# Kernel tuning notes

Measured on AMD Instinct MI355X. Metric: run time of the kernel, lower is better.

Reference implementation:

```python
import jax, jax.numpy as jnp
import numpy as np


def rotate_half(x):
    x1, x2 = jnp.split(x, 2, axis=-1)
    return jnp.concatenate((-x2, x1), axis=-1)


def setup_inputs() -> dict:
    key = jax.random.key(0)
    ks = jax.random.split(key, 8)
    B, S, H, C = 4, 2048, 2048, 512
    QK = H + C
    NH = 16
    dqk = QK // NH  # 160
    return {
        "hidden_states": jax.random.normal(ks[0], (B, S, H), jnp.float32),
        "cond_states": jax.random.normal(ks[1], (B, S, C), jnp.float32),
        "cos": jax.random.uniform(ks[2], (S, dqk), jnp.float32),
        "sin": jax.random.uniform(ks[3], (S, dqk), jnp.float32),
        "Wq": jax.random.normal(ks[4], (QK, QK), jnp.float32) * 0.02,
        "Wk": jax.random.normal(ks[5], (QK, QK), jnp.float32) * 0.02,
        "Wv": jax.random.normal(ks[6], (H, H), jnp.float32) * 0.02,
        "Wo": jax.random.normal(ks[7], (H, H), jnp.float32) * 0.02,
    }


def reference(hidden_states, cond_states, cos, sin, Wq, Wk, Wv, Wo):
    B, S, H = hidden_states.shape
    NH = 16
    qk_in = jnp.concatenate([hidden_states, cond_states], axis=-1)  # [B,S,QK]
    q = (qk_in @ Wq.T).reshape(B, S, NH, -1)  # [B,S,NH,dqk]
    k = (qk_in @ Wk.T).reshape(B, S, NH, -1)
    v = (hidden_states @ Wv.T).reshape(B, S, NH, -1)  # [B,S,NH,dv]
    # RoPE in fp32; cos/sin broadcast over batch and heads: (S,1,dqk)
    cos_b = cos[:, None, :].astype(jnp.float32)
    sin_b = sin[:, None, :].astype(jnp.float32)
    qf, kf = q.astype(jnp.float32), k.astype(jnp.float32)
    q = (qf * cos_b + rotate_half(qf) * sin_b).astype(q.dtype)
    k = (kf * cos_b + rotate_half(kf) * sin_b).astype(k.dtype)
    dqk = q.shape[-1]
    scale = 1.0 / jnp.sqrt(jnp.asarray(dqk, q.dtype))
    scores = jnp.einsum("bqhd,bkhd->bhqk", q, k) * scale  # [B,NH,S,S]
    probs = jax.nn.softmax(scores, axis=-1)
    attn = jnp.einsum("bhqk,bkhd->bqhd", probs, v)  # [B,S,NH,dv]
    attn = attn.reshape(B, S, -1)
    return attn @ Wo.T
```

## Files before the change

### kernel.cpp

```cpp
#include <hip/hip_runtime.h>
#include <cstdint>
#include <cstddef>

typedef __attribute__((ext_vector_type(8))) short bf16x8;
typedef __attribute__((ext_vector_type(4))) short bf16x4;
typedef __attribute__((ext_vector_type(4))) float f32x4;

#define MFMA_BF16 __builtin_amdgcn_mfma_f32_16x16x32_bf16

constexpr int B_   = 4;
constexpr int S_   = 2048;
constexpr int H_   = 2048;
constexpr int C_   = 512;
constexpr int QKD  = 2560;
constexpr int NH   = 16;
constexpr int DQK  = 160;
constexpr int DV   = 128;
constexpr int MTOT = B_ * S_;

static __device__ __forceinline__ short f2bf(float f) {
  unsigned u = __builtin_bit_cast(unsigned, f);
  u += 0x7FFFu + ((u >> 16) & 1u);
  return (short)(u >> 16);
}
static __device__ __forceinline__ float bf2f(short h) {
  unsigned u = ((unsigned)(unsigned short)h) << 16;
  return __builtin_bit_cast(float, u);
}
static __device__ __forceinline__ unsigned cvt_pk_bf16(float a, float b) {
  unsigned r;
  asm("v_cvt_pk_bf16_f32 %0, %1, %2" : "=v"(r) : "v"(a), "v"(b));
  return r;
}
static __device__ __forceinline__ void gload_lds16(const void* g, void* l) {
  __builtin_amdgcn_global_load_lds((const __attribute__((address_space(1))) unsigned*)g,
                                   (__attribute__((address_space(3))) unsigned*)l, 16, 0, 0);
}

__global__ __launch_bounds__(256) void k_build_qkin(const float* __restrict__ hidden,
                                                    const float* __restrict__ cond,
                                                    short* __restrict__ qk) {
  int i = blockIdx.x * 256 + threadIdx.x;
  int row = i / (QKD / 4);
  int c4  = i - row * (QKD / 4);
  f32x4 v;
  if (c4 < H_ / 4) v = *((const f32x4*)hidden + (size_t)row * (H_ / 4) + c4);
  else             v = *((const f32x4*)cond   + (size_t)row * (C_ / 4) + (c4 - H_ / 4));
  bf16x4 o;
  o[0] = f2bf(v[0]); o[1] = f2bf(v[1]); o[2] = f2bf(v[2]); o[3] = f2bf(v[3]);
  *(bf16x4*)(qk + (size_t)row * QKD + c4 * 4) = o;
}

__global__ __launch_bounds__(256) void k_cvt_bf16(const float* __restrict__ in,
                                                  short* __restrict__ out) {
  size_t i = (size_t)blockIdx.x * 256 + threadIdx.x;
  f32x4 v = *((const f32x4*)in + i);
  bf16x4 o;
  o[0] = f2bf(v[0]); o[1] = f2bf(v[1]); o[2] = f2bf(v[2]); o[3] = f2bf(v[3]);
  *(bf16x4*)(out + i * 4) = o;
}

template<int MODE>
__global__ __launch_bounds__(256) void k_gemm_bt(const short* __restrict__ A,
                                                 const short* __restrict__ W,
                                                 void* __restrict__ Cp,
                                                 int N, int K, int lda) {
  __shared__ short lA[128 * 32];
  __shared__ short lB[128 * 32];
  const int tid = threadIdx.x;
  const int lane = tid & 63, wid = tid >> 6;
  const int gx = gridDim.x, gy = gridDim.y;
  const int nwg = gx * gy, cpx = nwg >> 3;
  const int wg  = blockIdx.y * gx + blockIdx.x;
  const int wg2 = (wg & 7) * cpx + (wg >> 3);
  const int xb  = wg2 / gy, yb = wg2 - xb * gy;
  const int m0 = yb * 128, n0 = xb * 128;
  const int wr = wid >> 1, wc = wid & 1;
  const int l15 = lane & 15, l4 = lane >> 4;
  f32x4 acc[4][4] = {};

  const int srow = lane >> 2;
  const int scol = (lane & 3) * 8;
  const short* Abase = A + (size_t)m0 * lda;
  const short* Wbase = W + (size_t)n0 * K;
  const int nkt = K >> 5;

  for (int kt = 0; kt < nkt; ++kt) {
    const int k0 = kt << 5;
#pragma unroll
    for (int i = 0; i < 2; ++i) {
      int c = wid * 2 + i;
      gload_lds16(Abase + (size_t)(c * 16 + srow) * lda + k0 + scol, &lA[c * 512]);
      gload_lds16(Wbase + (size_t)(c * 16 + srow) * K   + k0 + scol, &lB[c * 512]);
    }
    __syncthreads();
    bf16x8 af[4], bv[4];
#pragma unroll
    for (int x = 0; x < 4; ++x) {
      af[x] = *(const bf16x8*)&lA[(wr * 64 + x * 16 + l15) * 32 + l4 * 8];
      bv[x] = *(const bf16x8*)&lB[(wc * 64 + x * 16 + l15) * 32 + l4 * 8];
    }
#pragma unroll
    for (int mi = 0; mi < 4; ++mi)
#pragma unroll
      for (int nj = 0; nj < 4; ++nj)
        acc[mi][nj] = MFMA_BF16(af[mi], bv[nj], acc[mi][nj], 0, 0, 0);
    __syncthreads();
  }

#pragma unroll
  for (int mi = 0; mi < 4; ++mi) {
#pragma unroll
    for (int nj = 0; nj < 4; ++nj) {
      int crow = m0 + wr * 64 + mi * 16 + l4 * 4;
      int ccol = n0 + wc * 64 + nj * 16 + l15;
      if constexpr (MODE == 0) {
        int b = crow >> 11;
        int s = crow - (b << 11);
        int h = ccol / DQK;
        int d = ccol - h * DQK;
        short* dst = (short*)Cp + ((size_t)(b * NH + h) * S_) * DQK + d;
#pragma unroll
        for (int r = 0; r < 4; ++r)
          dst[(size_t)(s + r) * DQK] = f2bf(acc[mi][nj][r]);
      } else if constexpr (MODE == 1) {
        int b = crow >> 11;
        int s = crow - (b << 11);
        int h = ccol >> 7;
        int d = ccol & 127;
        short* dst = (short*)Cp + ((size_t)(b * NH + h) * DV + d) * S_ + s;
        bf16x4 o;
        o[0] = f2bf(acc[mi][nj][0]); o[1] = f2bf(acc[mi][nj][1]);
        o[2] = f2bf(acc[mi][nj][2]); o[3] = f2bf(acc[mi][nj][3]);
        *(bf16x4*)dst = o;
      } else {
        float* dst = (float*)Cp + (size_t)crow * N + ccol;
#pragma unroll
        for (int r = 0; r < 4; ++r) dst[(size_t)r * N] = acc[mi][nj][r];
      }
    }
  }
}

__global__ __launch_bounds__(256) void k_rope(short* __restrict__ x,
                                              const float* __restrict__ cs,
                                              const float* __restrict__ sn) {
  int i = blockIdx.x * 256 + threadIdx.x;
  int c4   = i % 20;
  int rest = i / 20;
  int s  = rest & (S_ - 1);
  int bh = rest >> 11;
  size_t base = ((size_t)bh * S_ + s) * DQK;
  int d = c4 * 4;
  bf16x4 x1 = *(bf16x4*)(x + base + d);
  bf16x4 x2 = *(bf16x4*)(x + base + d + 80);
  f32x4 c1 = *(const f32x4*)(cs + (size_t)s * DQK + d);
  f32x4 s1 = *(const f32x4*)(sn + (size_t)s * DQK + d);
  f32x4 c2 = *(const f32x4*)(cs + (size_t)s * DQK + d + 80);
  f32x4 s2 = *(const f32x4*)(sn + (size_t)s * DQK + d + 80);
  bf16x4 o1, o2;
#pragma unroll
  for (int j = 0; j < 4; ++j) {
    float a = bf2f(x1[j]), b = bf2f(x2[j]);
    o1[j] = f2bf(a * c1[j] - b * s1[j]);
    o2[j] = f2bf(b * c2[j] + a * s2[j]);
  }
  *(bf16x4*)(x + base + d)      = o1;
  *(bf16x4*)(x + base + d + 80) = o2;
}

__global__ __launch_bounds__(256) void k_attn(const short* __restrict__ q,
                                              const short* __restrict__ k,
                                              const short* __restrict__ vt,
                                              short* __restrict__ attn) {
  __shared__ short lK[64 * 160];
  __shared__ short lV[128 * 64];
  __shared__ short lP[4 * 32 * 64];
  const int tid = threadIdx.x, lane = tid & 63, wid = tid >> 6;
  const int wg  = blockIdx.y * gridDim.x + blockIdx.x;
  const int wg2 = (wg & 7) * 128 + (wg >> 3);
  const int bh  = wg2 >> 4, b = bh >> 4, h = bh & 15;
  const int q0  = (wg2 & 15) * 128;
  const short* Q  = q  + (size_t)bh * S_ * DQK;
  const char*  Kb = (const char*)(k + (size_t)bh * S_ * DQK);
  const char*  Vb = (const char*)(vt + (size_t)bh * DV * S_);
  const int l15 = lane & 15, l4 = lane >> 4;

  bf16x8 qf[2][5];
#pragma unroll
  for (int mi = 0; mi < 2; ++mi)
#pragma unroll
    for (int ks = 0; ks < 5; ++ks)
      qf[mi][ks] = *(const bf16x8*)(Q + (size_t)(q0 + wid * 32 + mi * 16 + l15) * DQK + ks * 32 + l4 * 8);

  f32x4 acc[2][8] = {};
  float mrow[2], lrow[2];
#pragma unroll
  for (int mi = 0; mi < 2; ++mi) { mrow[mi] = -1e30f; lrow[mi] = 0.f; }
  const float csc = 0.07905694150420949f * 1.44269504089f;

  int koff[5], kcolS[5];
#pragma unroll
  for (int i = 0; i < 5; ++i) {
    int c = wid * 5 + i;
    int off = c * 1024 + lane * 16;
    int row = off / 320;
    int colB = off - row * 320;
    int g = colB >> 4;
    int colS = (g < 16) ? (colB ^ ((row & 7) << 4)) : (colB ^ ((row & 3) << 4));
    koff[i] = row;  kcolS[i] = colS;
  }

  for (int kv0 = 0; kv0 < S_; kv0 += 64) {
#pragma unroll
    for (int i = 0; i < 5; ++i)
      gload_lds16(Kb + (size_t)(kv0 + koff[i]) * 320 + kcolS[i], &lK[(wid * 5 + i) * 512]);
#pragma unroll
    for (int i = 0; i < 4; ++i) {
      int c = wid * 4 + i;
      int row = c * 8 + (lane >> 3);
      int cb  = (lane & 7) ^ (lane >> 3);
      gload_lds16(Vb + (size_t)row * (S_ * 2) + kv0 * 2 + cb * 16, &lV[c * 512]);
    }
    __syncthreads();

    f32x4 sc[4][2] = {};
#pragma unroll
    for (int kj = 0; kj < 4; ++kj) {
      int row = kj * 16 + l15;
      int x7 = (row & 7) << 4, x3 = (row & 3) << 4;
#pragma unroll
      for (int ks = 0; ks < 5; ++ks) {
        int colB = (ks < 4) ? ((ks * 64 + l4 * 16) ^ x7) : ((256 + l4 * 16) ^ x3);
        bf16x8 kf = *(const bf16x8*)((const char*)lK + row * 320 + colB);
        sc[kj][0] = MFMA_BF16(kf, qf[0][ks], sc[kj][0], 0, 0, 0);
        sc[kj][1] = MFMA_BF16(kf, qf[1][ks], sc[kj][1], 0, 0, 0);
      }
    }

    float pms[2];
#pragma unroll
    for (int mi = 0; mi < 2; ++mi) {
      float mv = sc[0][mi][0];
#pragma unroll
      for (int kj = 0; kj < 4; ++kj)
#pragma unroll
        for (int r = 0; r < 4; ++r) mv = fmaxf(mv, sc[kj][mi][r]);
      mv = fmaxf(mv, __shfl_xor(mv, 16, 64));
      mv = fmaxf(mv, __shfl_xor(mv, 32, 64));
      pms[mi] = mv * csc;
    }
    if (__any((pms[0] > mrow[0] + 8.0f) || (pms[1] > mrow[1] + 8.0f))) {
#pragma unroll
      for (int mi = 0; mi < 2; ++mi) {
        float mn = fmaxf(mrow[mi], pms[mi]);
        float al = exp2f(mrow[mi] - mn);
        mrow[mi] = mn; lrow[mi] *= al;
#pragma unroll
        for (int r = 0; r < 4; ++r) {
          float alr = __shfl(al, (lane & 48) | (l4 * 4 + r), 64);
#pragma unroll
          for (int nf = 0; nf < 8; ++nf) acc[mi][nf][r] *= alr;
        }
      }
    }
#pragma unroll
    for (int mi = 0; mi < 2; ++mi) {
      int qrow = mi * 16 + l15;
      char* lpb = (char*)lP + wid * 4096 + qrow * 128;
      int xq = (qrow & 7) << 4;
#pragma unroll
      for (int kj = 0; kj < 4; ++kj) {
        float p0 = exp2f(sc[kj][mi][0] * csc - mrow[mi]);
        float p1 = exp2f(sc[kj][mi][1] * csc - mrow[mi]);
        float p2 = exp2f(sc[kj][mi][2] * csc - mrow[mi]);
        float p3 = exp2f(sc[kj][mi][3] * csc - mrow[mi]);
        lrow[mi] += (p0 + p1) + (p2 + p3);
        uint2 w;
        w.x = cvt_pk_bf16(p0, p1);
        w.y = cvt_pk_bf16(p2, p3);
        *(uint2*)(lpb + ((kj * 32 + l4 * 8) ^ xq)) = w;
      }
    }

#pragma unroll
    for (int kc = 0; kc < 2; ++kc) {
      bf16x8 pa[2];
#pragma unroll
      for (int mi = 0; mi < 2; ++mi) {
        int row = mi * 16 + l15;
        pa[mi] = *(const bf16x8*)((const char*)lP + wid * 4096 + row * 128 +
                                  ((kc * 64 + l4 * 16) ^ ((row & 7) << 4)));
      }
#pragma unroll
      for (int nf = 0; nf < 8; ++nf) {
        int row = nf * 16 + l15;
        bf16x8 vf = *(const bf16x8*)((const char*)lV + row * 128 +
                                     ((kc * 64 + l4 * 16) ^ ((row & 7) << 4)));
        acc[0][nf] = MFMA_BF16(pa[0], vf, acc[0][nf], 0, 0, 0);
        acc[1][nf] = MFMA_BF16(pa[1], vf, acc[1][nf], 0, 0, 0);
      }
    }
    __syncthreads();
  }

  float invr[2][4];
#pragma unroll
  for (int mi = 0; mi < 2; ++mi) {
    float s = lrow[mi];
    s += __shfl_xor(s, 16, 64);
    s += __shfl_xor(s, 32, 64);
    float inv = 1.0f / s;
#pragma unroll
    for (int r = 0; r < 4; ++r)
      invr[mi][r] = __shfl(inv, (lane & 48) | (l4 * 4 + r), 64);
  }
#pragma unroll
  for (int mi = 0; mi < 2; ++mi)
#pragma unroll
    for (int nf = 0; nf < 8; ++nf) {
      size_t col = (size_t)h * DV + nf * 16 + l15;
#pragma unroll
      for (int r = 0; r < 4; ++r) {
        int mg = q0 + wid * 32 + mi * 16 + l4 * 4 + r;
        attn[(size_t)(b * S_ + mg) * H_ + col] = f2bf(acc[mi][nf][r] * invr[mi][r]);
      }
    }
}

extern "C" void kernel_launch(void* const* d_in, const int* in_sizes, int n_in,
                              void* d_out, int out_size, void* d_ws, size_t ws_size,
                              hipStream_t stream) {
  const float* hidden = (const float*)d_in[0];
  const float* cond   = (const float*)d_in[1];
  const float* cosp   = (const float*)d_in[2];
  const float* sinp   = (const float*)d_in[3];
  const float* Wq     = (const float*)d_in[4];
  const float* Wk     = (const float*)d_in[5];
  const float* Wv     = (const float*)d_in[6];
  const float* Wo     = (const float*)d_in[7];

  constexpr size_t SZ_QKIN = (size_t)MTOT * QKD * 2;
  constexpr size_t SZ_VT   = (size_t)MTOT * H_ * 2;
  constexpr size_t SZ_WBF  = (size_t)QKD * QKD * 2;
  constexpr size_t WS_NEED = SZ_QKIN * 3 + SZ_VT + SZ_WBF;
  if (ws_size < WS_NEED) return;

  char* ws = (char*)d_ws;
  short* qk_in = (short*)(ws);
  short* qbuf  = (short*)(ws + SZ_QKIN);
  short* kbuf  = (short*)(ws + 2 * SZ_QKIN);
  short* vtbuf = (short*)(ws + 3 * SZ_QKIN);
  short* w_bf  = (short*)(ws + 3 * SZ_QKIN + SZ_VT);
  short* attn  = qk_in;
  float* outp  = (float*)d_out;

  k_build_qkin<<<(MTOT * QKD / 4) / 256, 256, 0, stream>>>(hidden, cond, qk_in);

  dim3 gq(QKD / 128, MTOT / 128);
  dim3 gv(H_ / 128, MTOT / 128);

  k_cvt_bf16<<<(QKD * QKD / 4) / 256, 256, 0, stream>>>(Wq, w_bf);
  k_gemm_bt<0><<<gq, 256, 0, stream>>>(qk_in, w_bf, qbuf, QKD, QKD, QKD);

  k_cvt_bf16<<<(QKD * QKD / 4) / 256, 256, 0, stream>>>(Wk, w_bf);
  k_gemm_bt<0><<<gq, 256, 0, stream>>>(qk_in, w_bf, kbuf, QKD, QKD, QKD);

  k_cvt_bf16<<<(H_ * H_ / 4) / 256, 256, 0, stream>>>(Wv, w_bf);
  k_gemm_bt<1><<<gv, 256, 0, stream>>>(qk_in, w_bf, vtbuf, H_, H_, QKD);

  k_rope<<<(B_ * NH * S_ * 20) / 256, 256, 0, stream>>>(qbuf, cosp, sinp);
  k_rope<<<(B_ * NH * S_ * 20) / 256, 256, 0, stream>>>(kbuf, cosp, sinp);

  dim3 ga(S_ / 128, B_ * NH);
  k_attn<<<ga, 256, 0, stream>>>(qbuf, kbuf, vtbuf, attn);

  k_cvt_bf16<<<(H_ * H_ / 4) / 256, 256, 0, stream>>>(Wo, w_bf);
  k_gemm_bt<2><<<gv, 256, 0, stream>>>(attn, w_bf, outp, H_, H_, H_);
}
```

Measured before the change: 967.6 us.

## Double-buffer K tiles in attention and prefetch next tile during compute

The attention loop now keeps two LDS buffers for K. The next K tile is issued asynchronously while the current one is consumed, and a manual vmcnt wait before the PV MFMAs replaces the per-iteration barrier after the loads. The P staging buffer shrinks to a padded per-wave 32x40 layout and is written in halves just before each PV k-chunk. The MFMA sections are wrapped in s_setprio to favour matrix issue. Both the V tile and the prefetched K tile are written by all waves but only synchronised by per-wave vmcnt waits and the loop-end barrier, so cross-wave LDS visibility may be racy.

```diff
diff --git a/kernel.cpp b/kernel.cpp
--- a/kernel.cpp
+++ b/kernel.cpp
@@ -173,9 +173,9 @@
                                               const short* __restrict__ k,
                                               const short* __restrict__ vt,
                                               short* __restrict__ attn) {
-  __shared__ short lK[64 * 160];
+  __shared__ short lK[2][64 * 160];
   __shared__ short lV[128 * 64];
-  __shared__ short lP[4 * 32 * 64];
+  __shared__ short lP[4][32][40];
   const int tid = threadIdx.x, lane = tid & 63, wid = tid >> 6;
   const int wg  = blockIdx.y * gridDim.x + blockIdx.x;
   const int wg2 = (wg & 7) * 128 + (wg >> 3);
@@ -210,21 +210,31 @@
     int colS = (g < 16) ? (colB ^ ((row & 7) << 4)) : (colB ^ ((row & 3) << 4));
     koff[i] = row;  kcolS[i] = colS;
   }
-
-  for (int kv0 = 0; kv0 < S_; kv0 += 64) {
-#pragma unroll
-    for (int i = 0; i < 5; ++i)
-      gload_lds16(Kb + (size_t)(kv0 + koff[i]) * 320 + kcolS[i], &lK[(wid * 5 + i) * 512]);
+  const int vrow = lane >> 3;
+  const int vcb  = (lane & 7) ^ vrow;
+
+#pragma unroll
+  for (int i = 0; i < 5; ++i)
+    gload_lds16(Kb + (size_t)koff[i] * 320 + kcolS[i], &lK[0][(wid * 5 + i) * 512]);
+  __syncthreads();
+
+  int cur = 0;
+  for (int t = 0; t < 32; ++t, cur ^= 1) {
+    const int kv0 = t * 64;
 #pragma unroll
     for (int i = 0; i < 4; ++i) {
       int c = wid * 4 + i;
-      int row = c * 8 + (lane >> 3);
-      int cb  = (lane & 7) ^ (lane >> 3);
-      gload_lds16(Vb + (size_t)row * (S_ * 2) + kv0 * 2 + cb * 16, &lV[c * 512]);
-    }
-    __syncthreads();
+      gload_lds16(Vb + (size_t)(c * 8 + vrow) * (S_ * 2) + kv0 * 2 + vcb * 16, &lV[c * 512]);
+    }
+    {
+      const int kvn = ((t + 1) & 31) * 64;
+#pragma unroll
+      for (int i = 0; i < 5; ++i)
+        gload_lds16(Kb + (size_t)(kvn + koff[i]) * 320 + kcolS[i], &lK[cur ^ 1][(wid * 5 + i) * 512]);
+    }
 
     f32x4 sc[4][2] = {};
+    __builtin_amdgcn_s_setprio(1);
 #pragma unroll
     for (int kj = 0; kj < 4; ++kj) {
       int row = kj * 16 + l15;
@@ -232,11 +242,12 @@
 #pragma unroll
       for (int ks = 0; ks < 5; ++ks) {
         int colB = (ks < 4) ? ((ks * 64 + l4 * 16) ^ x7) : ((256 + l4 * 16) ^ x3);
-        bf16x8 kf = *(const bf16x8*)((const char*)lK + row * 320 + colB);
+        bf16x8 kf = *(const bf16x8*)((const char*)&lK[cur][0] + row * 320 + colB);
         sc[kj][0] = MFMA_BF16(kf, qf[0][ks], sc[kj][0], 0, 0, 0);
         sc[kj][1] = MFMA_BF16(kf, qf[1][ks], sc[kj][1], 0, 0, 0);
       }
     }
+    __builtin_amdgcn_s_setprio(0);
 
     float pms[2];
 #pragma unroll
@@ -264,11 +275,9 @@
         }
       }
     }
+    uint2 pk[2][4];
 #pragma unroll
     for (int mi = 0; mi < 2; ++mi) {
-      int qrow = mi * 16 + l15;
-      char* lpb = (char*)lP + wid * 4096 + qrow * 128;
-      int xq = (qrow & 7) << 4;
 #pragma unroll
       for (int kj = 0; kj < 4; ++kj) {
         float p0 = exp2f(sc[kj][mi][0] * csc - mrow[mi]);
@@ -276,22 +285,27 @@
         float p2 = exp2f(sc[kj][mi][2] * csc - mrow[mi]);
         float p3 = exp2f(sc[kj][mi][3] * csc - mrow[mi]);
         lrow[mi] += (p0 + p1) + (p2 + p3);
-        uint2 w;
-        w.x = cvt_pk_bf16(p0, p1);
-        w.y = cvt_pk_bf16(p2, p3);
-        *(uint2*)(lpb + ((kj * 32 + l4 * 8) ^ xq)) = w;
-      }
-    }
-
+        pk[mi][kj].x = cvt_pk_bf16(p0, p1);
+        pk[mi][kj].y = cvt_pk_bf16(p2, p3);
+      }
+    }
+
+    __builtin_amdgcn_s_setprio(1);
 #pragma unroll
     for (int kc = 0; kc < 2; ++kc) {
+#pragma unroll
+      for (int mi = 0; mi < 2; ++mi) {
+        int qrow = mi * 16 + l15;
+#pragma unroll
+        for (int j2 = 0; j2 < 2; ++j2)
+          *(uint2*)&lP[wid][qrow][j2 * 16 + l4 * 4] = pk[mi][kc * 2 + j2];
+      }
       bf16x8 pa[2];
 #pragma unroll
-      for (int mi = 0; mi < 2; ++mi) {
-        int row = mi * 16 + l15;
-        pa[mi] = *(const bf16x8*)((const char*)lP + wid * 4096 + row * 128 +
-                                  ((kc * 64 + l4 * 16) ^ ((row & 7) << 4)));
-      }
+      for (int mi = 0; mi < 2; ++mi)
+        pa[mi] = *(const bf16x8*)&lP[wid][mi * 16 + l15][l4 * 8];
+      if (kc == 0)
+        asm volatile("s_waitcnt vmcnt(5)" ::: "memory");
 #pragma unroll
       for (int nf = 0; nf < 8; ++nf) {
         int row = nf * 16 + l15;
@@ -301,6 +315,7 @@
         acc[1][nf] = MFMA_BF16(pa[1], vf, acc[1][nf], 0, 0, 0);
       }
     }
+    __builtin_amdgcn_s_setprio(0);
     __syncthreads();
   }
 
```

Result: no change. 972.8 us (+0.5%).

## Restructure attention to 8 waves of 16 query rows with setprio

Applied to the files above, without the earlier changes.

The attention kernel now runs 512 threads per block, with each of the 8 waves handling 16 query rows instead of 32. This halves per-wave registers (Q fragments, accumulators) so more waves can be resident, and the K/V tile loads are spread across twice as many waves. The P tile is staged in a smaller padded LDS buffer per 32-column chunk, and s_setprio raises wave priority around the MFMA regions. The trade-off is that each K/V fragment read from LDS now feeds half as many MFMAs, which lowers reuse per LDS read.

```diff
diff --git a/kernel.cpp b/kernel.cpp
--- a/kernel.cpp
+++ b/kernel.cpp
@@ -169,15 +169,15 @@
   *(bf16x4*)(x + base + d + 80) = o2;
 }
 
-__global__ __launch_bounds__(256) void k_attn(const short* __restrict__ q,
-                                              const short* __restrict__ k,
-                                              const short* __restrict__ vt,
-                                              short* __restrict__ attn) {
+__global__ __launch_bounds__(512, 4) void k_attn(const short* __restrict__ q,
+                                                 const short* __restrict__ k,
+                                                 const short* __restrict__ vt,
+                                                 short* __restrict__ attn) {
   __shared__ short lK[64 * 160];
   __shared__ short lV[128 * 64];
-  __shared__ short lP[4 * 32 * 64];
+  __shared__ short lP[8][16][40];
   const int tid = threadIdx.x, lane = tid & 63, wid = tid >> 6;
-  const int wg  = blockIdx.y * gridDim.x + blockIdx.x;
+  const int wg  = blockIdx.x;
   const int wg2 = (wg & 7) * 128 + (wg >> 3);
   const int bh  = wg2 >> 4, b = bh >> 4, h = bh & 15;
   const int q0  = (wg2 & 15) * 128;
@@ -186,23 +186,19 @@
   const char*  Vb = (const char*)(vt + (size_t)bh * DV * S_);
   const int l15 = lane & 15, l4 = lane >> 4;
 
-  bf16x8 qf[2][5];
-#pragma unroll
-  for (int mi = 0; mi < 2; ++mi)
-#pragma unroll
-    for (int ks = 0; ks < 5; ++ks)
-      qf[mi][ks] = *(const bf16x8*)(Q + (size_t)(q0 + wid * 32 + mi * 16 + l15) * DQK + ks * 32 + l4 * 8);
-
-  f32x4 acc[2][8] = {};
-  float mrow[2], lrow[2];
-#pragma unroll
-  for (int mi = 0; mi < 2; ++mi) { mrow[mi] = -1e30f; lrow[mi] = 0.f; }
+  bf16x8 qf[5];
+#pragma unroll
+  for (int ks = 0; ks < 5; ++ks)
+    qf[ks] = *(const bf16x8*)(Q + (size_t)(q0 + wid * 16 + l15) * DQK + ks * 32 + l4 * 8);
+
+  f32x4 acc[8] = {};
+  float mrow = -1e30f, lrow = 0.f;
   const float csc = 0.07905694150420949f * 1.44269504089f;
 
-  int koff[5], kcolS[5];
-#pragma unroll
-  for (int i = 0; i < 5; ++i) {
-    int c = wid * 5 + i;
+  int koff[3], kcolS[3];
+#pragma unroll
+  for (int i = 0; i < 3; ++i) {
+    int c = (i < 2) ? (i * 8 + wid) : (16 + wid);
     int off = c * 1024 + lane * 16;
     int row = off / 320;
     int colB = off - row * 320;
@@ -210,21 +206,23 @@
     int colS = (g < 16) ? (colB ^ ((row & 7) << 4)) : (colB ^ ((row & 3) << 4));
     koff[i] = row;  kcolS[i] = colS;
   }
+  const int vrow = lane >> 3;
+  const int vcb  = (lane & 7) ^ vrow;
 
   for (int kv0 = 0; kv0 < S_; kv0 += 64) {
-#pragma unroll
-    for (int i = 0; i < 5; ++i)
-      gload_lds16(Kb + (size_t)(kv0 + koff[i]) * 320 + kcolS[i], &lK[(wid * 5 + i) * 512]);
-#pragma unroll
-    for (int i = 0; i < 4; ++i) {
-      int c = wid * 4 + i;
-      int row = c * 8 + (lane >> 3);
-      int cb  = (lane & 7) ^ (lane >> 3);
-      gload_lds16(Vb + (size_t)row * (S_ * 2) + kv0 * 2 + cb * 16, &lV[c * 512]);
+    gload_lds16(Kb + (size_t)(kv0 + koff[0]) * 320 + kcolS[0], &lK[(wid)      * 512]);
+    gload_lds16(Kb + (size_t)(kv0 + koff[1]) * 320 + kcolS[1], &lK[(8 + wid)  * 512]);
+    if (wid < 4)
+      gload_lds16(Kb + (size_t)(kv0 + koff[2]) * 320 + kcolS[2], &lK[(16 + wid) * 512]);
+#pragma unroll
+    for (int i = 0; i < 2; ++i) {
+      int c = wid * 2 + i;
+      gload_lds16(Vb + (size_t)(c * 8 + vrow) * (S_ * 2) + kv0 * 2 + vcb * 16, &lV[c * 512]);
     }
     __syncthreads();
 
-    f32x4 sc[4][2] = {};
+    f32x4 sc[4] = {};
+    __builtin_amdgcn_s_setprio(1);
 #pragma unroll
     for (int kj = 0; kj < 4; ++kj) {
       int row = kj * 16 + l15;
@@ -233,99 +231,78 @@
       for (int ks = 0; ks < 5; ++ks) {
         int colB = (ks < 4) ? ((ks * 64 + l4 * 16) ^ x7) : ((256 + l4 * 16) ^ x3);
         bf16x8 kf = *(const bf16x8*)((const char*)lK + row * 320 + colB);
-        sc[kj][0] = MFMA_BF16(kf, qf[0][ks], sc[kj][0], 0, 0, 0);
-        sc[kj][1] = MFMA_BF16(kf, qf[1][ks], sc[kj][1], 0, 0, 0);
+        sc[kj] = MFMA_BF16(kf, qf[ks], sc[kj], 0, 0, 0);
       }
     }
-
-    float pms[2];
-#pragma unroll
-    for (int mi = 0; mi < 2; ++mi) {
-      float mv = sc[0][mi][0];
-#pragma unroll
-      for (int kj = 0; kj < 4; ++kj)
-#pragma unroll
-        for (int r = 0; r < 4; ++r) mv = fmaxf(mv, sc[kj][mi][r]);
-      mv = fmaxf(mv, __shfl_xor(mv, 16, 64));
-      mv = fmaxf(mv, __shfl_xor(mv, 32, 64));
-      pms[mi] = mv * csc;
-    }
-    if (__any((pms[0] > mrow[0] + 8.0f) || (pms[1] > mrow[1] + 8.0f))) {
-#pragma unroll
-      for (int mi = 0; mi < 2; ++mi) {
-        float mn = fmaxf(mrow[mi], pms[mi]);
-        float al = exp2f(mrow[mi] - mn);
-        mrow[mi] = mn; lrow[mi] *= al;
-#pragma unroll
-        for (int r = 0; r < 4; ++r) {
-          float alr = __shfl(al, (lane & 48) | (l4 * 4 + r), 64);
-#pragma unroll
-          for (int nf = 0; nf < 8; ++nf) acc[mi][nf][r] *= alr;
-        }
+    __builtin_amdgcn_s_setprio(0);
+
+    float mv = sc[0][0];
+#pragma unroll
+    for (int kj = 0; kj < 4; ++kj)
+#pragma unroll
+      for (int r = 0; r < 4; ++r) mv = fmaxf(mv, sc[kj][r]);
+    mv = fmaxf(mv, __shfl_xor(mv, 16, 64));
+    mv = fmaxf(mv, __shfl_xor(mv, 32, 64));
+    float pms = mv * csc;
+    if (__any(pms > mrow + 8.0f)) {
+      float mn = fmaxf(mrow, pms);
+      float al = exp2f(mrow - mn);
+      mrow = mn; lrow *= al;
+#pragma unroll
+      for (int r = 0; r < 4; ++r) {
+        float alr = __shfl(al, (lane & 48) | (l4 * 4 + r), 64);
+#pragma unroll
+        for (int nf = 0; nf < 8; ++nf) acc[nf][r] *= alr;
       }
     }
-#pragma unroll
-    for (int mi = 0; mi < 2; ++mi) {
-      int qrow = mi * 16 + l15;
-      char* lpb = (char*)lP + wid * 4096 + qrow * 128;
-      int xq = (qrow & 7) << 4;
-#pragma unroll
-      for (int kj = 0; kj < 4; ++kj) {
-        float p0 = exp2f(sc[kj][mi][0] * csc - mrow[mi]);
-        float p1 = exp2f(sc[kj][mi][1] * csc - mrow[mi]);
-        float p2 = exp2f(sc[kj][mi][2] * csc - mrow[mi]);
-        float p3 = exp2f(sc[kj][mi][3] * csc - mrow[mi]);
-        lrow[mi] += (p0 + p1) + (p2 + p3);
-        uint2 w;
-        w.x = cvt_pk_bf16(p0, p1);
-        w.y = cvt_pk_bf16(p2, p3);
-        *(uint2*)(lpb + ((kj * 32 + l4 * 8) ^ xq)) = w;
-      }
-    }
-
+    uint2 pk[4];
+#pragma unroll
+    for (int kj = 0; kj < 4; ++kj) {
+      float p0 = exp2f(sc[kj][0] * csc - mrow);
+      float p1 = exp2f(sc[kj][1] * csc - mrow);
+      float p2 = exp2f(sc[kj][2] * csc - mrow);
+      float p3 = exp2f(sc[kj][3] * csc - mrow);
+      lrow += (p0 + p1) + (p2 + p3);
+      pk[kj].x = cvt_pk_bf16(p0, p1);
+      pk[kj].y = cvt_pk_bf16(p2, p3);
+    }
+
+    __builtin_amdgcn_s_setprio(1);
 #pragma unroll
     for (int kc = 0; kc < 2; ++kc) {
-      bf16x8 pa[2];
-#pragma unroll
-      for (int mi = 0; mi < 2; ++mi) {
-        int row = mi * 16 + l15;
-        pa[mi] = *(const bf16x8*)((const char*)lP + wid * 4096 + row * 128 +
-                                  ((kc * 64 + l4 * 16) ^ ((row & 7) << 4)));
-      }
+#pragma unroll
+      for (int j2 = 0; j2 < 2; ++j2)
+        *(uint2*)&lP[wid][l15][j2 * 16 + l4 * 4] = pk[kc * 2 + j2];
+      bf16x8 pa = *(const bf16x8*)&lP[wid][l15][l4 * 8];
 #pragma unroll
       for (int nf = 0; nf < 8; ++nf) {
         int row = nf * 16 + l15;
         bf16x8 vf = *(const bf16x8*)((const char*)lV + row * 128 +
                                      ((kc * 64 + l4 * 16) ^ ((row & 7) << 4)));
-        acc[0][nf] = MFMA_BF16(pa[0], vf, acc[0][nf], 0, 0, 0);
-        acc[1][nf] = MFMA_BF16(pa[1], vf, acc[1][nf], 0, 0, 0);
+        acc[nf] = MFMA_BF16(pa, vf, acc[nf], 0, 0, 0);
       }
     }
+    __builtin_amdgcn_s_setprio(0);
     __syncthreads();
   }
 
-  float invr[2][4];
-#pragma unroll
-  for (int mi = 0; mi < 2; ++mi) {
-    float s = lrow[mi];
-    s += __shfl_xor(s, 16, 64);
-    s += __shfl_xor(s, 32, 64);
-    float inv = 1.0f / s;
-#pragma unroll
-    for (int r = 0; r < 4; ++r)
-      invr[mi][r] = __shfl(inv, (lane & 48) | (l4 * 4 + r), 64);
-  }
-#pragma unroll
-  for (int mi = 0; mi < 2; ++mi)
-#pragma unroll
-    for (int nf = 0; nf < 8; ++nf) {
-      size_t col = (size_t)h * DV + nf * 16 + l15;
-#pragma unroll
-      for (int r = 0; r < 4; ++r) {
-        int mg = q0 + wid * 32 + mi * 16 + l4 * 4 + r;
-        attn[(size_t)(b * S_ + mg) * H_ + col] = f2bf(acc[mi][nf][r] * invr[mi][r]);
-      }
-    }
+  float s = lrow;
+  s += __shfl_xor(s, 16, 64);
+  s += __shfl_xor(s, 32, 64);
+  float inv = 1.0f / s;
+  float invr[4];
+#pragma unroll
+  for (int r = 0; r < 4; ++r)
+    invr[r] = __shfl(inv, (lane & 48) | (l4 * 4 + r), 64);
+#pragma unroll
+  for (int nf = 0; nf < 8; ++nf) {
+    size_t col = (size_t)h * DV + nf * 16 + l15;
+#pragma unroll
+    for (int r = 0; r < 4; ++r) {
+      int mg = q0 + wid * 16 + l4 * 4 + r;
+      attn[(size_t)(b * S_ + mg) * H_ + col] = f2bf(acc[nf][r] * invr[r]);
+    }
+  }
 }
 
 extern "C" void kernel_launch(void* const* d_in, const int* in_sizes, int n_in,
@@ -372,8 +349,7 @@
   k_rope<<<(B_ * NH * S_ * 20) / 256, 256, 0, stream>>>(qbuf, cosp, sinp);
   k_rope<<<(B_ * NH * S_ * 20) / 256, 256, 0, stream>>>(kbuf, cosp, sinp);
 
-  dim3 ga(S_ / 128, B_ * NH);
-  k_attn<<<ga, 256, 0, stream>>>(qbuf, kbuf, vtbuf, attn);
+  k_attn<<<1024, 512, 0, stream>>>(qbuf, kbuf, vtbuf, attn);
 
   k_cvt_bf16<<<(H_ * H_ / 4) / 256, 256, 0, stream>>>(Wo, w_bf);
   k_gemm_bt<2><<<gv, 256, 0, stream>>>(attn, w_bf, outp, H_, H_, H_);
```

New measurement: 871.6 us. 1.11x faster.
